# Optimization experiments

Measured on AMD Instinct MI355X. Metric: run time of the kernel, lower is better.

## Reference

```python
import jax, jax.numpy as jnp
import numpy as np

# dims: batch, samples, agents, obs_dim, action_dim, hidden
B, S, N, D, A, H = 512, 64, 8, 64, 16, 256
IN_DIM = (D + A) * N  # 640


def mish(x):
    return x * jnp.tanh(jax.nn.softplus(x))


def setup_inputs() -> dict:
    key = jax.random.key(0)
    ks = jax.random.split(key, 9)
    u = lambda k, shape, fan_in: jax.random.uniform(
        k, shape, jnp.float32, -1.0 / np.sqrt(fan_in), 1.0 / np.sqrt(fan_in))
    return {
        "state": jax.random.normal(ks[0], (B, N, D), jnp.float32),
        "action": jax.random.normal(ks[1], (B, N, A), jnp.float32),
        "W1": u(ks[2], (IN_DIM, H), IN_DIM),
        "b1": u(ks[3], (H,), IN_DIM),
        "W2": u(ks[4], (H, H), H),
        "b2": u(ks[5], (H,), H),
        "W3": u(ks[6], (H, 1), H),
        "b3": u(ks[7], (1,), H),
        # random grand-coalition permutations of the N agents, per (batch, sample)
        "perm": jnp.argsort(jax.random.uniform(ks[8], (B, S, N)), axis=-1).astype(jnp.int32),
    }


def reference(state, action, W1, b1, W2, b2, W3, b3, perm):
    # subcoalition mask [B,S,N,N]: torch builds one-hot(perm) @ tril(ones),
    # i.e. mask[b,s,i,j] = 1 iff j <= perm[b,s,i]
    subcoal = (jnp.arange(N) <= perm[..., None]).astype(state.dtype)
    # gathered actions in coalition order [B,S,N,A]: act_g[b,s,j] = action[b, perm[b,s,j]]
    act_g = action[jnp.arange(B)[:, None, None], perm]
    # masked subcoalition actions [B,S,N,N,A] -> [B,S,N,N*A]
    act = (act_g[:, :, None, :, :] * subcoal[..., None]).reshape(B, S, N, N * A)
    # flattened global obs broadcast over (sample, agent) axes [B,S,N,N*D]
    obs = jnp.broadcast_to(state.reshape(B, 1, 1, N * D), (B, S, N, N * D))
    x = jnp.concatenate([obs, act], axis=-1)  # [B,S,N,IN_DIM]
    # per-agent loop in torch uses shared q1 weights -> single batched MLP
    h = mish(x @ W1 + b1)
    h = mish(h @ W2 + b2)
    q = h @ W3 + b3                   # [B,S,N,1]
    q1 = q.mean(axis=1).squeeze(-1)   # mean over samples -> [B,N]
    return (q1, q1)
```

## Files before the change

### kernel.cpp

```cpp
#include <hip/hip_runtime.h>

typedef unsigned short ushort_t;
typedef __attribute__((ext_vector_type(8))) short short8;
typedef __attribute__((ext_vector_type(4))) float floatx4;


__device__ __forceinline__ float mish_f(float x) {
    float e = __expf(x);
    float w = fmaf(e, e + 2.0f, 2.0f);
    return x - 2.0f * x * __builtin_amdgcn_rcpf(w);
}

__device__ __forceinline__ unsigned f2bf_u(float f) {
    unsigned int u = __float_as_uint(f);
    return (u + 0x7fffu + ((u >> 16) & 1u)) >> 16;
}

__global__ __launch_bounds__(256) void prep_kernel(
        const float* __restrict__ state,
        const float* __restrict__ action,
        const float* __restrict__ W1,
        const float* __restrict__ b1,
        const float* __restrict__ W2,
        float* __restrict__ obsW,
        float* __restrict__ actW,
        ushort_t* __restrict__ W2T) {
    int bid = blockIdx.x;
    int t = threadIdx.x;
    if (bid < 512) {
        int b = bid;
        const float* stp = state + (size_t)b * 512;
        const float* acp = action + (size_t)b * 128;

        float a0 = 0.f, a1 = 0.f, a2 = 0.f, a3 = 0.f;
#pragma unroll 8
        for (int f = 0; f < 512; f += 4) {
            a0 = fmaf(stp[f + 0], W1[(f + 0) * 256 + t], a0);
            a1 = fmaf(stp[f + 1], W1[(f + 1) * 256 + t], a1);
            a2 = fmaf(stp[f + 2], W1[(f + 2) * 256 + t], a2);
            a3 = fmaf(stp[f + 3], W1[(f + 3) * 256 + t], a3);
        }
        obsW[b * 256 + t] = (a0 + a1) + (a2 + a3) + b1[t];

        const float* W1a = W1 + 512 * 256;
        for (int j = 0; j < 8; ++j) {
            float acc[8];
#pragma unroll
            for (int n = 0; n < 8; ++n) acc[n] = 0.f;
#pragma unroll
            for (int a = 0; a < 16; ++a) {
                float w = W1a[(j * 16 + a) * 256 + t];
#pragma unroll
                for (int n = 0; n < 8; ++n)
                    acc[n] = fmaf(acp[n * 16 + a], w, acc[n]);
            }
#pragma unroll
            for (int n = 0; n < 8; ++n)
                actW[(((size_t)b * 8 + n) * 8 + j) * 256 + t] = acc[n];
        }
    } else {
        int n = (bid - 512) * 4 + (t >> 6);
        int klo = (t & 63);
        for (int kk = 0; kk < 4; ++kk) {
            int k = kk * 64 + klo;
            W2T[n * 256 + k] = (ushort_t)f2bf_u(W2[k * 256 + n]);
        }
    }
}

#define LDK 264

__global__ __launch_bounds__(256, 4) void main_kernel(
        const float* __restrict__ obsW, const float* __restrict__ actW,
        const ushort_t* __restrict__ W2T, const int* __restrict__ perm,
        const float* __restrict__ b2,
        const float* __restrict__ W3, const float* __restrict__ b3,
        float* __restrict__ qk) {
    __shared__ ushort_t h1[64 * LDK];
    __shared__ float obsb[256];
    __shared__ int perm_s[64];
    __shared__ float qpart[4][64];

    int t = threadIdx.x;
    int bid = blockIdx.x;
    int b = bid >> 3;
    int sg = bid & 7;
    int s0 = sg * 8;

    obsb[t] = obsW[b * 256 + t];
    if (t < 64) perm_s[t] = perm[((size_t)b * 64 + s0) * 8 + t];
    __syncthreads();

    const float* actb = actW + (size_t)b * 64 * 256;
    {
        int half = t >> 7;
        int c = (t & 127) * 2;
        float ob0 = obsb[c], ob1 = obsb[c + 1];
#pragma unroll
        for (int sl2 = 0; sl2 < 4; ++sl2) {
            int sl = half * 4 + sl2;
            float r0 = ob0, r1 = ob1;
#pragma unroll
            for (int j = 0; j < 8; ++j) {
                int p = perm_s[sl * 8 + j];
                float2 av = *reinterpret_cast<const float2*>(actb + (p * 8 + j) * 256 + c);
                r0 += av.x;
                r1 += av.y;
                unsigned pk = f2bf_u(mish_f(r0)) | (f2bf_u(mish_f(r1)) << 16);
                *reinterpret_cast<unsigned*>(&h1[(sl * 8 + j) * LDK + c]) = pk;
            }
        }
    }
    __syncthreads();

    int w = t >> 6;
    int lo = t & 15;
    int q = (t >> 4) & 3;

    floatx4 acc[4][4];
#pragma unroll
    for (int mt = 0; mt < 4; ++mt)
#pragma unroll
        for (int nt = 0; nt < 4; ++nt)
            acc[mt][nt] = (floatx4){0.f, 0.f, 0.f, 0.f};

    const ushort_t* w2base = W2T + ((size_t)(w * 64 + lo)) * 256 + q * 8;

#pragma unroll
    for (int ks = 0; ks < 8; ++ks) {
        short8 afr[4];
#pragma unroll
        for (int mt = 0; mt < 4; ++mt)
            afr[mt] = *reinterpret_cast<const short8*>(&h1[(mt * 16 + lo) * LDK + ks * 32 + q * 8]);
        short8 bfr[4];
#pragma unroll
        for (int nt = 0; nt < 4; ++nt)
            bfr[nt] = *reinterpret_cast<const short8*>(w2base + nt * 16 * 256 + ks * 32);
#pragma unroll
        for (int mt = 0; mt < 4; ++mt)
#pragma unroll
            for (int nt = 0; nt < 4; ++nt)
                acc[mt][nt] = __builtin_amdgcn_mfma_f32_16x16x32_bf16(afr[mt], bfr[nt], acc[mt][nt], 0, 0, 0);
    }

    float b2c[4], w3c[4];
#pragma unroll
    for (int nt = 0; nt < 4; ++nt) {
        int col = w * 64 + nt * 16 + lo;
        b2c[nt] = b2[col];
        w3c[nt] = W3[col];
    }
#pragma unroll
    for (int mt = 0; mt < 4; ++mt) {
        float part[4] = {0.f, 0.f, 0.f, 0.f};
#pragma unroll
        for (int nt = 0; nt < 4; ++nt) {
#pragma unroll
            for (int r = 0; r < 4; ++r) {
                float h2 = mish_f(acc[mt][nt][r] + b2c[nt]);
                part[r] = fmaf(h2, w3c[nt], part[r]);
            }
        }
#pragma unroll
        for (int r = 0; r < 4; ++r) {
            float v = part[r];
            v += __shfl_xor(v, 1);
            v += __shfl_xor(v, 2);
            v += __shfl_xor(v, 4);
            v += __shfl_xor(v, 8);
            if (lo == 0) qpart[w][mt * 16 + q * 4 + r] = v;
        }
    }
    __syncthreads();
    if (t < 64) {
        float qv = qpart[0][t] + qpart[1][t] + qpart[2][t] + qpart[3][t] + b3[0];
        qk[((size_t)b * 64 + s0) * 8 + t] = qv;
    }
}

__global__ __launch_bounds__(256) void final_kernel(
        const float* __restrict__ qk,
        const int* __restrict__ perm,
        float* __restrict__ out) {
    __shared__ float qs[4][512];
    __shared__ int ps[4][512];
    int t = threadIdx.x;
    int w = t >> 6;
    int lane = t & 63;
    int b = blockIdx.x * 4 + w;
    for (int r = 0; r < 8; ++r) {
        qs[w][r * 64 + lane] = qk[(size_t)b * 512 + r * 64 + lane];
        ps[w][r * 64 + lane] = perm[(size_t)b * 512 + r * 64 + lane];
    }
    __syncthreads();
    int i = lane & 7;
    int s0 = lane >> 3;
    float v = 0.0f;
    for (int s = s0; s < 64; s += 8) v += qs[w][s * 8 + ps[w][s * 8 + i]];
    v += __shfl_xor(v, 8);
    v += __shfl_xor(v, 16);
    v += __shfl_xor(v, 32);
    if (lane < 8) {
        float r = v * (1.0f / 64.0f);
        out[b * 8 + i] = r;
        out[4096 + b * 8 + i] = r;
    }
}

extern "C" void kernel_launch(void* const* d_in, const int* in_sizes, int n_in,
                              void* d_out, int out_size, void* d_ws, size_t ws_size,
                              hipStream_t stream) {
    const float* state  = (const float*)d_in[0];
    const float* action = (const float*)d_in[1];
    const float* W1     = (const float*)d_in[2];
    const float* b1     = (const float*)d_in[3];
    const float* W2     = (const float*)d_in[4];
    const float* b2     = (const float*)d_in[5];
    const float* W3     = (const float*)d_in[6];
    const float* b3     = (const float*)d_in[7];
    const int*   perm   = (const int*)d_in[8];
    float* out = (float*)d_out;

    char* ws = (char*)d_ws;
    float*    obsW = (float*)ws;
    float*    actW = (float*)(ws + 524288);
    ushort_t* W2T  = (ushort_t*)(ws + 524288 + 33554432);
    float*    qk   = (float*)(ws + 524288 + 33554432 + 131072);

    prep_kernel<<<576, 256, 0, stream>>>(state, action, W1, b1, W2, obsW, actW, W2T);
    main_kernel<<<4096, 256, 0, stream>>>(obsW, actW, W2T, perm, b2, W3, b3, qk);
    final_kernel<<<128, 256, 0, stream>>>(qk, perm, out);
}
```

Before: 198.8 us.

## Store actW in bf16, split prep work finer, and remap main-kernel block order

```diff
diff --git a/kernel.cpp b/kernel.cpp
--- a/kernel.cpp
+++ b/kernel.cpp
@@ -1,4 +1,5 @@
 #include <hip/hip_runtime.h>
+#include <hip/hip_bf16.h>
 
 typedef unsigned short ushort_t;
 typedef __attribute__((ext_vector_type(8))) short short8;
@@ -20,46 +21,47 @@
         const float* __restrict__ state,
         const float* __restrict__ action,
         const float* __restrict__ W1,
-        const float* __restrict__ b1,
         const float* __restrict__ W2,
         float* __restrict__ obsW,
-        float* __restrict__ actW,
+        ushort_t* __restrict__ actW,
         ushort_t* __restrict__ W2T) {
     int bid = blockIdx.x;
     int t = threadIdx.x;
-    if (bid < 512) {
-        int b = bid;
-        const float* stp = state + (size_t)b * 512;
-        const float* acp = action + (size_t)b * 128;
-
+    if (bid < 2048) {
+        int b = bid >> 2;
+        int kc = bid & 3;
+        const float* stp = state + (size_t)b * 512 + kc * 128;
+        const float* w1p = W1 + (size_t)(kc * 128) * 256 + t;
         float a0 = 0.f, a1 = 0.f, a2 = 0.f, a3 = 0.f;
 #pragma unroll 8
-        for (int f = 0; f < 512; f += 4) {
-            a0 = fmaf(stp[f + 0], W1[(f + 0) * 256 + t], a0);
-            a1 = fmaf(stp[f + 1], W1[(f + 1) * 256 + t], a1);
-            a2 = fmaf(stp[f + 2], W1[(f + 2) * 256 + t], a2);
-            a3 = fmaf(stp[f + 3], W1[(f + 3) * 256 + t], a3);
-        }
-        obsW[b * 256 + t] = (a0 + a1) + (a2 + a3) + b1[t];
-
-        const float* W1a = W1 + 512 * 256;
-        for (int j = 0; j < 8; ++j) {
-            float acc[8];
-#pragma unroll
-            for (int n = 0; n < 8; ++n) acc[n] = 0.f;
-#pragma unroll
-            for (int a = 0; a < 16; ++a) {
-                float w = W1a[(j * 16 + a) * 256 + t];
-#pragma unroll
-                for (int n = 0; n < 8; ++n)
-                    acc[n] = fmaf(acp[n * 16 + a], w, acc[n]);
-            }
+        for (int f = 0; f < 128; f += 4) {
+            a0 = fmaf(stp[f + 0], w1p[(f + 0) * 256], a0);
+            a1 = fmaf(stp[f + 1], w1p[(f + 1) * 256], a1);
+            a2 = fmaf(stp[f + 2], w1p[(f + 2) * 256], a2);
+            a3 = fmaf(stp[f + 3], w1p[(f + 3) * 256], a3);
+        }
+        atomicAdd(&obsW[b * 256 + t], (a0 + a1) + (a2 + a3));
+    } else if (bid < 6144) {
+        int idx = bid - 2048;
+        int b = idx >> 3;
+        int j = idx & 7;
+        const float* acp = action + (size_t)b * 128;
+        const float* W1a = W1 + (size_t)(512 + j * 16) * 256;
+        float acc[8];
+#pragma unroll
+        for (int n = 0; n < 8; ++n) acc[n] = 0.f;
+#pragma unroll
+        for (int a = 0; a < 16; ++a) {
+            float w = W1a[a * 256 + t];
 #pragma unroll
             for (int n = 0; n < 8; ++n)
-                actW[(((size_t)b * 8 + n) * 8 + j) * 256 + t] = acc[n];
-        }
+                acc[n] = fmaf(acp[n * 16 + a], w, acc[n]);
+        }
+#pragma unroll
+        for (int n = 0; n < 8; ++n)
+            actW[(((size_t)b * 8 + n) * 8 + j) * 256 + t] = (ushort_t)f2bf_u(acc[n]);
     } else {
-        int n = (bid - 512) * 4 + (t >> 6);
+        int n = (bid - 6144) * 4 + (t >> 6);
         int klo = (t & 63);
         for (int kk = 0; kk < 4; ++kk) {
             int k = kk * 64 + klo;
@@ -71,9 +73,9 @@
 #define LDK 264
 
 __global__ __launch_bounds__(256, 4) void main_kernel(
-        const float* __restrict__ obsW, const float* __restrict__ actW,
+        const float* __restrict__ obsW, const ushort_t* __restrict__ actW,
         const ushort_t* __restrict__ W2T, const int* __restrict__ perm,
-        const float* __restrict__ b2,
+        const float* __restrict__ b1, const float* __restrict__ b2,
         const float* __restrict__ W3, const float* __restrict__ b3,
         float* __restrict__ qk) {
     __shared__ ushort_t h1[64 * LDK];
@@ -83,15 +85,15 @@
 
     int t = threadIdx.x;
     int bid = blockIdx.x;
-    int b = bid >> 3;
-    int sg = bid & 7;
+    int b = (bid & 7) * 64 + ((bid >> 3) & 63);
+    int sg = bid >> 9;
     int s0 = sg * 8;
 
-    obsb[t] = obsW[b * 256 + t];
+    obsb[t] = obsW[b * 256 + t] + b1[t];
     if (t < 64) perm_s[t] = perm[((size_t)b * 64 + s0) * 8 + t];
     __syncthreads();
 
-    const float* actb = actW + (size_t)b * 64 * 256;
+    const ushort_t* actb = actW + (size_t)b * 64 * 256;
     {
         int half = t >> 7;
         int c = (t & 127) * 2;
@@ -99,15 +101,19 @@
 #pragma unroll
         for (int sl2 = 0; sl2 < 4; ++sl2) {
             int sl = half * 4 + sl2;
-            float r0 = ob0, r1 = ob1;
+            unsigned av[8];
 #pragma unroll
             for (int j = 0; j < 8; ++j) {
                 int p = perm_s[sl * 8 + j];
-                float2 av = *reinterpret_cast<const float2*>(actb + (p * 8 + j) * 256 + c);
-                r0 += av.x;
-                r1 += av.y;
-                unsigned pk = f2bf_u(mish_f(r0)) | (f2bf_u(mish_f(r1)) << 16);
-                *reinterpret_cast<unsigned*>(&h1[(sl * 8 + j) * LDK + c]) = pk;
+                av[j] = *reinterpret_cast<const unsigned*>(actb + (p * 8 + j) * 256 + c);
+            }
+            float r0 = ob0, r1 = ob1;
+#pragma unroll
+            for (int j = 0; j < 8; ++j) {
+                r0 += __uint_as_float(av[j] << 16);
+                r1 += __uint_as_float(av[j] & 0xffff0000u);
+                __hip_bfloat162 pk = __float22bfloat162_rn(make_float2(mish_f(r0), mish_f(r1)));
+                *reinterpret_cast<__hip_bfloat162*>(&h1[(sl * 8 + j) * LDK + c]) = pk;
             }
         }
     }
@@ -223,11 +229,12 @@
 
     char* ws = (char*)d_ws;
     float*    obsW = (float*)ws;
-    float*    actW = (float*)(ws + 524288);
-    ushort_t* W2T  = (ushort_t*)(ws + 524288 + 33554432);
-    float*    qk   = (float*)(ws + 524288 + 33554432 + 131072);
-
-    prep_kernel<<<576, 256, 0, stream>>>(state, action, W1, b1, W2, obsW, actW, W2T);
-    main_kernel<<<4096, 256, 0, stream>>>(obsW, actW, W2T, perm, b2, W3, b3, qk);
+    ushort_t* actW = (ushort_t*)(ws + 524288);
+    ushort_t* W2T  = (ushort_t*)(ws + 524288 + 16777216);
+    float*    qk   = (float*)(ws + 524288 + 16777216 + 131072);
+
+    hipMemsetAsync(obsW, 0, 512 * 256 * sizeof(float), stream);
+    prep_kernel<<<6208, 256, 0, stream>>>(state, action, W1, W2, obsW, actW, W2T);
+    main_kernel<<<4096, 256, 0, stream>>>(obsW, actW, W2T, perm, b1, b2, W3, b3, qk);
     final_kernel<<<128, 256, 0, stream>>>(qk, perm, out);
 }
```

Result: faster. 184.8 us (-7.0%).
